# Optimization experiments

Hardware: AMD Instinct MI355X
Metric: run time of the kernel (lower is better)

The kernel has to match this reference:

```python
import jax, jax.numpy as jnp
import numpy as np

N_NODES = 100000
N_EDGES = 1600000
IN_DIM, HIDDEN, OUT_DIM = 128, 64, 32


def setup_inputs() -> dict:
    key = jax.random.key(0)
    k1, k2, k3, k4 = jax.random.split(key, 4)
    x = jax.random.normal(k1, (N_NODES, IN_DIM), dtype=jnp.float32)
    # Glorot-style init for the two GCN linear layers
    W1 = jax.random.normal(k2, (IN_DIM, HIDDEN), dtype=jnp.float32) * (1.0 / np.sqrt(IN_DIM))
    b1 = jnp.zeros((HIDDEN,), dtype=jnp.float32)
    W2 = jax.random.normal(k3, (HIDDEN, OUT_DIM), dtype=jnp.float32) * (1.0 / np.sqrt(HIDDEN))
    b2 = jnp.zeros((OUT_DIM,), dtype=jnp.float32)
    edge_index = jax.random.randint(k4, (2, N_EDGES), 0, N_NODES, dtype=jnp.int32)
    return {"x": x, "W1": W1, "b1": b1, "W2": W2, "b2": b2, "edge_index": edge_index}


def _gcn_norm(edge_index, n_nodes):
    # Add self-loops and compute symmetric normalization D^{-1/2} (A+I) D^{-1/2}
    loops = jnp.arange(n_nodes, dtype=edge_index.dtype)
    src = jnp.concatenate([edge_index[0], loops])  # [E+N]
    dst = jnp.concatenate([edge_index[1], loops])
    deg = jax.ops.segment_sum(jnp.ones_like(dst, dtype=jnp.float32), dst,
                              num_segments=n_nodes)
    dinv = jnp.where(deg > 0, jax.lax.rsqrt(deg), 0.0)
    norm = dinv[src] * dinv[dst]  # [E+N]
    return src, dst, norm


def _gcn_conv(h, W, b, src, dst, norm, n_nodes):
    h = h @ W                                   # [N, out] linear transform first
    msg = h[src] * norm[:, None]                # gather + per-edge scale
    agg = jax.ops.segment_sum(msg, dst, num_segments=n_nodes)  # scatter-add
    return agg + b


def reference(x, W1, b1, W2, b2, edge_index):
    n = x.shape[0]
    src, dst, norm = _gcn_norm(edge_index, n)
    h = jax.nn.relu(_gcn_conv(x, W1, b1, src, dst, norm, n))
    # dropout is identity in eval mode (deterministic reference)
    z = _gcn_conv(h, W2, b2, src, dst, norm, n)
    return z
```

## Files before the change

### kernel.cpp

```cpp
#include <hip/hip_runtime.h>
#include <hip/hip_fp16.h>

#define NB_MAX 784
#define CAP    2560
#define CHUNK  8192

typedef _Float16 half8 __attribute__((ext_vector_type(8)));
typedef float f32x4_t __attribute__((ext_vector_type(4)));

__global__ __launch_bounds__(256) void k_bin_gemm1(
        const int* __restrict__ src, const int* __restrict__ dst,
        int* __restrict__ gcur, int* __restrict__ binned, int nb, int e,
        const float* __restrict__ x, const float* __restrict__ W1,
        __half* __restrict__ hp, int n, int binb) {
    __shared__ __align__(16) char smem[64 * 136 * 2];
    const int t = threadIdx.x;

    if (blockIdx.x < binb) {
        int* hist = (int*)smem;
        int* curs = hist + NB_MAX;
        const int base = blockIdx.x * CHUNK;
        const int lim = min(CHUNK, e - base);

        for (int i = t; i < NB_MAX; i += 256) hist[i] = 0;
        __syncthreads();

        const int i4lim = lim >> 2;
        for (int i = t; i < i4lim; i += 256) {
            int4 d = ((const int4*)(dst + base))[i];
            atomicAdd(&hist[d.x >> 7], 1);
            atomicAdd(&hist[d.y >> 7], 1);
            atomicAdd(&hist[d.z >> 7], 1);
            atomicAdd(&hist[d.w >> 7], 1);
        }
        for (int i = (i4lim << 2) + t; i < lim; i += 256)
            atomicAdd(&hist[dst[base + i] >> 7], 1);
        __syncthreads();

        for (int b = t; b < nb; b += 256) {
            int h = hist[b];
            curs[b] = h ? atomicAdd(&gcur[b], h) : 0;
        }
        __syncthreads();

        for (int i = t; i < i4lim; i += 256) {
            int4 d = ((const int4*)(dst + base))[i];
            int4 s = ((const int4*)(src + base))[i];
            int o0 = atomicAdd(&curs[d.x >> 7], 1);
            int o1 = atomicAdd(&curs[d.y >> 7], 1);
            int o2 = atomicAdd(&curs[d.z >> 7], 1);
            int o3 = atomicAdd(&curs[d.w >> 7], 1);
            if (o0 < CAP) binned[(size_t)(d.x >> 7) * CAP + o0] = (s.x << 7) | (d.x & 127);
            if (o1 < CAP) binned[(size_t)(d.y >> 7) * CAP + o1] = (s.y << 7) | (d.y & 127);
            if (o2 < CAP) binned[(size_t)(d.z >> 7) * CAP + o2] = (s.z << 7) | (d.z & 127);
            if (o3 < CAP) binned[(size_t)(d.w >> 7) * CAP + o3] = (s.w << 7) | (d.w & 127);
        }
        for (int i = (i4lim << 2) + t; i < lim; i += 256) {
            int d = dst[base + i], s = src[base + i];
            int off = atomicAdd(&curs[d >> 7], 1);
            if (off < CAP) binned[(size_t)(d >> 7) * CAP + off] = (s << 7) | (d & 127);
        }
        return;
    }

    _Float16* wt = (_Float16*)smem;

    for (int i = t; i < 128 * 64; i += 256) {
        int k = i >> 6, o = i & 63;
        wt[o * 136 + k] = (_Float16)W1[i];
    }
    __syncthreads();

    const int lane = t & 63;
    const int wid  = t >> 6;
    const int row0 = (blockIdx.x - binb) * 64 + wid * 16;
    const int rA   = lane & 15;
    const int g    = lane >> 4;

    f32x4_t acc0 = {0.f, 0.f, 0.f, 0.f};
    f32x4_t acc1 = {0.f, 0.f, 0.f, 0.f};
    f32x4_t acc2 = {0.f, 0.f, 0.f, 0.f};
    f32x4_t acc3 = {0.f, 0.f, 0.f, 0.f};

    const int arow = min(row0 + rA, n - 1);
    const float* ap0 = x + (size_t)arow * 128 + g * 8;

#pragma unroll
    for (int ks = 0; ks < 4; ++ks) {
        const float* ap = ap0 + ks * 32;
        float4 a0 = *(const float4*)ap;
        float4 a1 = *(const float4*)(ap + 4);
        half8 af;
        af[0] = (_Float16)a0.x; af[1] = (_Float16)a0.y;
        af[2] = (_Float16)a0.z; af[3] = (_Float16)a0.w;
        af[4] = (_Float16)a1.x; af[5] = (_Float16)a1.y;
        af[6] = (_Float16)a1.z; af[7] = (_Float16)a1.w;

        const _Float16* wb = wt + rA * 136 + ks * 32 + g * 8;
        half8 b0 = *(const half8*)(wb);
        half8 b1 = *(const half8*)(wb + 16 * 136);
        half8 b2 = *(const half8*)(wb + 32 * 136);
        half8 b3 = *(const half8*)(wb + 48 * 136);
        acc0 = __builtin_amdgcn_mfma_f32_16x16x32_f16(af, b0, acc0, 0, 0, 0);
        acc1 = __builtin_amdgcn_mfma_f32_16x16x32_f16(af, b1, acc1, 0, 0, 0);
        acc2 = __builtin_amdgcn_mfma_f32_16x16x32_f16(af, b2, acc2, 0, 0, 0);
        acc3 = __builtin_amdgcn_mfma_f32_16x16x32_f16(af, b3, acc3, 0, 0, 0);
    }

    _Float16* hph = (_Float16*)hp;
#pragma unroll
    for (int r = 0; r < 4; ++r) {
        int node = row0 + g * 4 + r;
        if (node >= n) continue;
        _Float16* o = hph + (size_t)node * 64 + rA;
        o[0]  = (_Float16)acc0[r];
        o[16] = (_Float16)acc1[r];
        o[32] = (_Float16)acc2[r];
        o[48] = (_Float16)acc3[r];
    }
}

__global__ __launch_bounds__(1024) void k_base(const int* __restrict__ gcur,
                                               int* __restrict__ cbase,
                                               int* __restrict__ rpx,
                                               int nb, int n, int e) {
    __shared__ int sm[1024];
    int t = threadIdx.x;
    int v = (t < nb) ? gcur[t] : 0;
    sm[t] = v;
    __syncthreads();
    for (int o = 1; o < 1024; o <<= 1) {
        int add = (t >= o) ? sm[t - o] : 0;
        __syncthreads();
        sm[t] += add;
        __syncthreads();
    }
    if (t < nb) cbase[t] = sm[t] - v;
    if (t == 0) rpx[n] = e;
}

__global__ __launch_bounds__(256) void k_sort(const int* __restrict__ binned,
                                              const int* __restrict__ gcur,
                                              const int* __restrict__ cbase,
                                              int* __restrict__ csr,
                                              int* __restrict__ rpx,
                                              float* __restrict__ dinv, int n) {
    __shared__ int hist[128], offs[128];
    const int t = threadIdx.x;
    const int b = blockIdx.x;
    if (t < 128) hist[t] = 0;
    __syncthreads();

    int sz = gcur[b];
    if (sz > CAP) sz = CAP;
    const int* bp = binned + (size_t)b * CAP;

    const int i4 = sz >> 2;
    for (int i = t; i < i4; i += 256) {
        int4 p = ((const int4*)bp)[i];
        atomicAdd(&hist[p.x & 127], 1);
        atomicAdd(&hist[p.y & 127], 1);
        atomicAdd(&hist[p.z & 127], 1);
        atomicAdd(&hist[p.w & 127], 1);
    }
    for (int i = (i4 << 2) + t; i < sz; i += 256)
        atomicAdd(&hist[bp[i] & 127], 1);
    __syncthreads();

    if (t < 128) offs[t] = hist[t];
    __syncthreads();
    for (int o = 1; o < 128; o <<= 1) {
        int add = (t < 128 && t >= o) ? offs[t - o] : 0;
        __syncthreads();
        if (t < 128) offs[t] += add;
        __syncthreads();
    }

    const int base = cbase[b];
    if (t < 128) {
        int node = (b << 7) + t;
        if (node < n) {
            rpx[node]  = base + offs[t] - hist[t];
            dinv[node] = rsqrtf(1.0f + (float)hist[t]);
        }
    }
    __syncthreads();
    if (t < 128) hist[t] = offs[t] - hist[t];
    __syncthreads();

    for (int i = t; i < sz; i += 256) {
        int p = bp[i];
        int pos = base + atomicAdd(&hist[p & 127], 1);
        csr[pos] = p >> 7;
    }
}


union Pk8 { float4 f4; __half2 h2[4]; };

__device__ inline void addrow(float acc[8], float4 v) {
    Pk8 u; u.f4 = v;
#pragma unroll
    for (int j = 0; j < 4; ++j) {
        float2 t = __half22float2(u.h2[j]);
        acc[2 * j]     += t.x;
        acc[2 * j + 1] += t.y;
    }
}

__device__ inline void addrow_s(float acc[8], float4 v, float s) {
    Pk8 u; u.f4 = v;
#pragma unroll
    for (int j = 0; j < 4; ++j) {
        float2 t = __half22float2(u.h2[j]);
        acc[2 * j]     = fmaf(t.x, s, acc[2 * j]);
        acc[2 * j + 1] = fmaf(t.y, s, acc[2 * j + 1]);
    }
}

__global__ __launch_bounds__(256) void k_agg1(const int* __restrict__ rpx,
                                              const int* __restrict__ csr,
                                              const __half* __restrict__ hp,
                                              const float* __restrict__ dinv,
                                              const float* __restrict__ b1,
                                              const float* __restrict__ W2,
                                              __half* __restrict__ hp2, int n) {
    __shared__ float w2t[32 * 68];
    __shared__ float tl[32 * 68];
    const int t = threadIdx.x;

    for (int i = t; i < 64 * 32; i += 256) {
        int f = i >> 5, j = i & 31;
        w2t[j * 68 + f] = W2[i];
    }

    const int nl   = t >> 3;
    const int q    = t & 7;
    const int node = blockIdx.x * 32 + nl;
    const bool alive = node < n;

    float acc[8];
#pragma unroll
    for (int j = 0; j < 8; ++j) acc[j] = 0.f;

    float di = 0.f;
    if (alive) {
        const float4* hp4 = (const float4*)hp;
        int start = rpx[node], end = rpx[node + 1];
        di = dinv[node];
        addrow_s(acc, hp4[(size_t)node * 8 + q], di);

        int p = start;
        for (; p + 8 <= end; p += 8) {
            int s[8];
#pragma unroll
            for (int j = 0; j < 8; ++j) s[j] = csr[p + j];
            float ds[8];
#pragma unroll
            for (int j = 0; j < 8; ++j) ds[j] = dinv[s[j]];
            float4 v[8];
#pragma unroll
            for (int j = 0; j < 8; ++j) v[j] = hp4[(size_t)s[j] * 8 + q];
#pragma unroll
            for (int j = 0; j < 8; ++j) addrow_s(acc, v[j], ds[j]);
        }
        for (; p + 2 <= end; p += 2) {
            int s0 = csr[p], s1 = csr[p + 1];
            float d0 = dinv[s0], d1 = dinv[s1];
            float4 v0 = hp4[(size_t)s0 * 8 + q];
            float4 v1 = hp4[(size_t)s1 * 8 + q];
            addrow_s(acc, v0, d0);
            addrow_s(acc, v1, d1);
        }
        if (p < end) {
            int s0 = csr[p];
            addrow_s(acc, hp4[(size_t)s0 * 8 + q], dinv[s0]);
        }
    }

    float4 ba = ((const float4*)b1)[q * 2];
    float4 bb = ((const float4*)b1)[q * 2 + 1];
    float4 t0, t1;
    t0.x = fmaxf(fmaf(acc[0], di, ba.x), 0.f);
    t0.y = fmaxf(fmaf(acc[1], di, ba.y), 0.f);
    t0.z = fmaxf(fmaf(acc[2], di, ba.z), 0.f);
    t0.w = fmaxf(fmaf(acc[3], di, ba.w), 0.f);
    t1.x = fmaxf(fmaf(acc[4], di, bb.x), 0.f);
    t1.y = fmaxf(fmaf(acc[5], di, bb.y), 0.f);
    t1.z = fmaxf(fmaf(acc[6], di, bb.z), 0.f);
    t1.w = fmaxf(fmaf(acc[7], di, bb.w), 0.f);
    *(float4*)(tl + nl * 68 + q * 8)     = t0;
    *(float4*)(tl + nl * 68 + q * 8 + 4) = t1;
    __syncthreads();

    if (!alive) return;

    const float* trow = tl + nl * 68;
    const float* wa = w2t + q * 68;
    const float* wb = w2t + (q + 8) * 68;
    const float* wc = w2t + (q + 16) * 68;
    const float* wd = w2t + (q + 24) * 68;
    float o0 = 0.f, o1 = 0.f, o2 = 0.f, o3 = 0.f;
#pragma unroll
    for (int f4 = 0; f4 < 16; ++f4) {
        float4 tv = *(const float4*)(trow + f4 * 4);
        float4 v0 = *(const float4*)(wa + f4 * 4);
        float4 v1 = *(const float4*)(wb + f4 * 4);
        float4 v2 = *(const float4*)(wc + f4 * 4);
        float4 v3 = *(const float4*)(wd + f4 * 4);
        o0 += tv.x * v0.x + tv.y * v0.y + tv.z * v0.z + tv.w * v0.w;
        o1 += tv.x * v1.x + tv.y * v1.y + tv.z * v1.z + tv.w * v1.w;
        o2 += tv.x * v2.x + tv.y * v2.y + tv.z * v2.z + tv.w * v2.w;
        o3 += tv.x * v3.x + tv.y * v3.y + tv.z * v3.z + tv.w * v3.w;
    }
    _Float16* hq = (_Float16*)hp2 + (size_t)node * 32;
    hq[q]      = (_Float16)(o0 * di);
    hq[q + 8]  = (_Float16)(o1 * di);
    hq[q + 16] = (_Float16)(o2 * di);
    hq[q + 24] = (_Float16)(o3 * di);
}

template<int LOGF>
__global__ __launch_bounds__(256) void k_aggregate(const int* __restrict__ rpx,
                                                   const int* __restrict__ csr,
                                                   const __half* __restrict__ hp,
                                                   const float* __restrict__ dinv,
                                                   const float* __restrict__ bias,
                                                   float* __restrict__ out, int n) {
    constexpr int F   = 1 << LOGF;
    constexpr int TPN = F / 8;
    int gid  = blockIdx.x * 256 + threadIdx.x;
    int node = gid / TPN;
    int q    = gid % TPN;
    if (node >= n) return;

    const float4* hp4 = (const float4*)hp;
    int start = rpx[node], end = rpx[node + 1];

    float acc[8];
#pragma unroll
    for (int j = 0; j < 8; ++j) acc[j] = 0.f;
    addrow(acc, hp4[(size_t)node * TPN + q]);

    int p = start;
    for (; p + 8 <= end; p += 8) {
        int s[8];
#pragma unroll
        for (int j = 0; j < 8; ++j) s[j] = csr[p + j];
        float4 v[8];
#pragma unroll
        for (int j = 0; j < 8; ++j) v[j] = hp4[(size_t)s[j] * TPN + q];
#pragma unroll
        for (int j = 0; j < 8; ++j) addrow(acc, v[j]);
    }
    for (; p + 2 <= end; p += 2) {
        int s0 = csr[p], s1 = csr[p + 1];
        float4 v0 = hp4[(size_t)s0 * TPN + q];
        float4 v1 = hp4[(size_t)s1 * TPN + q];
        addrow(acc, v0);
        addrow(acc, v1);
    }
    if (p < end)
        addrow(acc, hp4[(size_t)csr[p] * TPN + q]);

    float di = dinv[node];
    float4 b0 = ((const float4*)bias)[q * 2];
    float4 b1v = ((const float4*)bias)[q * 2 + 1];
    float4 r0, r1;
    r0.x = fmaf(acc[0], di, b0.x); r0.y = fmaf(acc[1], di, b0.y);
    r0.z = fmaf(acc[2], di, b0.z); r0.w = fmaf(acc[3], di, b0.w);
    r1.x = fmaf(acc[4], di, b1v.x); r1.y = fmaf(acc[5], di, b1v.y);
    r1.z = fmaf(acc[6], di, b1v.z); r1.w = fmaf(acc[7], di, b1v.w);
    float4* o4 = (float4*)out;
    o4[(size_t)node * (F / 4) + q * 2]     = r0;
    o4[(size_t)node * (F / 4) + q * 2 + 1] = r1;
}


extern "C" void kernel_launch(void* const* d_in, const int* in_sizes, int n_in,
                              void* d_out, int out_size, void* d_ws, size_t ws_size,
                              hipStream_t stream) {
    const float* x  = (const float*)d_in[0];
    const float* W1 = (const float*)d_in[1];
    const float* b1 = (const float*)d_in[2];
    const float* W2 = (const float*)d_in[3];
    const float* b2 = (const float*)d_in[4];
    const int*   ei = (const int*)d_in[5];

    const int N = in_sizes[0] / 128;
    const int E = in_sizes[5] / 2;
    const int* src = ei;
    const int* dst = ei + E;
    const int NB = (N + 127) >> 7;

    char* w = (char*)d_ws;
    int*    gcur   = (int*)w;                  w += NB_MAX * 4;
    int*    cbase  = (int*)w;                  w += NB_MAX * 4;
    int*    rpx    = (int*)w;                  w += (size_t)(N + 4) * 4;
    float*  dinv   = (float*)w;                w += (size_t)N * 4;
    int*    binned = (int*)w;                  w += (size_t)NB_MAX * CAP * 4;
    int*    csr    = (int*)w;                  w += (size_t)E * 4;
    __half* hp     = (__half*)w;               w += (size_t)N * 64 * 2;
    __half* hp2    = (__half*)w;               w += (size_t)N * 32 * 2;
    float*  out    = (float*)d_out;

    const int binb = (E + CHUNK - 1) / CHUNK;
    const int gb1  = (N + 63) / 64;

    hipMemsetAsync(gcur, 0, NB_MAX * 4, stream);

    k_bin_gemm1<<<binb + gb1, 256, 0, stream>>>(src, dst, gcur, binned, NB, E,
                                                x, W1, hp, N, binb);

    k_base<<<1, 1024, 0, stream>>>(gcur, cbase, rpx, NB, N, E);
    k_sort<<<NB, 256, 0, stream>>>(binned, gcur, cbase, csr, rpx, dinv, N);

    k_agg1<<<(N + 31) / 32, 256, 0, stream>>>(rpx, csr, hp, dinv, b1, W2, hp2, N);

    k_aggregate<5><<<(N * 4 + 255) / 256, 256, 0, stream>>>(rpx, csr, hp2, dinv, b2, out, N);
}
```

Before: 136.4 us.

## Fold bin prefix scan into sort kernel and use nontemporal streaming loads

Removes the separate single-block prefix-scan kernel. Each sort block now sums the counts of all preceding bins itself with a block reduction, which saves one kernel launch and its serialization point at the cost of some redundant reads of the small count array. It also switches streaming reads of edge, bin and CSR data, plus the final output stores, to nontemporal loads and stores to reduce cache pollution.

Result: slower. 146.3 us (+7.2%).

```diff
diff --git a/kernel.cpp b/kernel.cpp
--- a/kernel.cpp
+++ b/kernel.cpp
@@ -7,6 +7,10 @@
 
 typedef _Float16 half8 __attribute__((ext_vector_type(8)));
 typedef float f32x4_t __attribute__((ext_vector_type(4)));
+typedef int   i32x4   __attribute__((ext_vector_type(4)));
+
+__device__ inline int   ntld (const int*   p) { return __builtin_nontemporal_load(p); }
+__device__ inline i32x4 ntld4(const int*   p) { return __builtin_nontemporal_load((const i32x4*)p); }
 
 __global__ __launch_bounds__(256) void k_bin_gemm1(
         const int* __restrict__ src, const int* __restrict__ dst,
@@ -44,8 +48,8 @@
         __syncthreads();
 
         for (int i = t; i < i4lim; i += 256) {
-            int4 d = ((const int4*)(dst + base))[i];
-            int4 s = ((const int4*)(src + base))[i];
+            i32x4 d = ntld4(dst + base + i * 4);
+            i32x4 s = ntld4(src + base + i * 4);
             int o0 = atomicAdd(&curs[d.x >> 7], 1);
             int o1 = atomicAdd(&curs[d.y >> 7], 1);
             int o2 = atomicAdd(&curs[d.z >> 7], 1);
@@ -120,36 +124,28 @@
     }
 }
 
-__global__ __launch_bounds__(1024) void k_base(const int* __restrict__ gcur,
-                                               int* __restrict__ cbase,
-                                               int* __restrict__ rpx,
-                                               int nb, int n, int e) {
-    __shared__ int sm[1024];
-    int t = threadIdx.x;
-    int v = (t < nb) ? gcur[t] : 0;
-    sm[t] = v;
-    __syncthreads();
-    for (int o = 1; o < 1024; o <<= 1) {
-        int add = (t >= o) ? sm[t - o] : 0;
-        __syncthreads();
-        sm[t] += add;
-        __syncthreads();
-    }
-    if (t < nb) cbase[t] = sm[t] - v;
-    if (t == 0) rpx[n] = e;
-}
-
 __global__ __launch_bounds__(256) void k_sort(const int* __restrict__ binned,
                                               const int* __restrict__ gcur,
-                                              const int* __restrict__ cbase,
                                               int* __restrict__ csr,
                                               int* __restrict__ rpx,
-                                              float* __restrict__ dinv, int n) {
+                                              float* __restrict__ dinv,
+                                              int n, int e) {
     __shared__ int hist[128], offs[128];
+    __shared__ int red[256];
     const int t = threadIdx.x;
     const int b = blockIdx.x;
+
+    int partial = 0;
+    for (int j = t; j < b; j += 256) partial += gcur[j];
+    red[t] = partial;
     if (t < 128) hist[t] = 0;
     __syncthreads();
+    for (int o = 128; o > 0; o >>= 1) {
+        if (t < o) red[t] += red[t + o];
+        __syncthreads();
+    }
+    const int base = red[0];
+    if (b == 0 && t == 0) rpx[n] = e;
 
     int sz = gcur[b];
     if (sz > CAP) sz = CAP;
@@ -157,14 +153,14 @@
 
     const int i4 = sz >> 2;
     for (int i = t; i < i4; i += 256) {
-        int4 p = ((const int4*)bp)[i];
+        i32x4 p = ntld4(bp + i * 4);
         atomicAdd(&hist[p.x & 127], 1);
         atomicAdd(&hist[p.y & 127], 1);
         atomicAdd(&hist[p.z & 127], 1);
         atomicAdd(&hist[p.w & 127], 1);
     }
     for (int i = (i4 << 2) + t; i < sz; i += 256)
-        atomicAdd(&hist[bp[i] & 127], 1);
+        atomicAdd(&hist[ntld(bp + i) & 127], 1);
     __syncthreads();
 
     if (t < 128) offs[t] = hist[t];
@@ -176,7 +172,6 @@
         __syncthreads();
     }
 
-    const int base = cbase[b];
     if (t < 128) {
         int node = (b << 7) + t;
         if (node < n) {
@@ -189,7 +184,7 @@
     __syncthreads();
 
     for (int i = t; i < sz; i += 256) {
-        int p = bp[i];
+        int p = ntld(bp + i);
         int pos = base + atomicAdd(&hist[p & 127], 1);
         csr[pos] = p >> 7;
     }
@@ -254,7 +249,7 @@
         for (; p + 8 <= end; p += 8) {
             int s[8];
 #pragma unroll
-            for (int j = 0; j < 8; ++j) s[j] = csr[p + j];
+            for (int j = 0; j < 8; ++j) s[j] = ntld(csr + p + j);
             float ds[8];
 #pragma unroll
             for (int j = 0; j < 8; ++j) ds[j] = dinv[s[j]];
@@ -265,7 +260,7 @@
             for (int j = 0; j < 8; ++j) addrow_s(acc, v[j], ds[j]);
         }
         for (; p + 2 <= end; p += 2) {
-            int s0 = csr[p], s1 = csr[p + 1];
+            int s0 = ntld(csr + p), s1 = ntld(csr + p + 1);
             float d0 = dinv[s0], d1 = dinv[s1];
             float4 v0 = hp4[(size_t)s0 * 8 + q];
             float4 v1 = hp4[(size_t)s1 * 8 + q];
@@ -273,7 +268,7 @@
             addrow_s(acc, v1, d1);
         }
         if (p < end) {
-            int s0 = csr[p];
+            int s0 = ntld(csr + p);
             addrow_s(acc, hp4[(size_t)s0 * 8 + q], dinv[s0]);
         }
     }
@@ -346,7 +341,7 @@
     for (; p + 8 <= end; p += 8) {
         int s[8];
 #pragma unroll
-        for (int j = 0; j < 8; ++j) s[j] = csr[p + j];
+        for (int j = 0; j < 8; ++j) s[j] = ntld(csr + p + j);
         float4 v[8];
 #pragma unroll
         for (int j = 0; j < 8; ++j) v[j] = hp4[(size_t)s[j] * TPN + q];
@@ -354,26 +349,26 @@
         for (int j = 0; j < 8; ++j) addrow(acc, v[j]);
     }
     for (; p + 2 <= end; p += 2) {
-        int s0 = csr[p], s1 = csr[p + 1];
+        int s0 = ntld(csr + p), s1 = ntld(csr + p + 1);
         float4 v0 = hp4[(size_t)s0 * TPN + q];
         float4 v1 = hp4[(size_t)s1 * TPN + q];
         addrow(acc, v0);
         addrow(acc, v1);
     }
     if (p < end)
-        addrow(acc, hp4[(size_t)csr[p] * TPN + q]);
+        addrow(acc, hp4[(size_t)ntld(csr + p) * TPN + q]);
 
     float di = dinv[node];
     float4 b0 = ((const float4*)bias)[q * 2];
     float4 b1v = ((const float4*)bias)[q * 2 + 1];
-    float4 r0, r1;
+    f32x4_t r0, r1;
     r0.x = fmaf(acc[0], di, b0.x); r0.y = fmaf(acc[1], di, b0.y);
     r0.z = fmaf(acc[2], di, b0.z); r0.w = fmaf(acc[3], di, b0.w);
     r1.x = fmaf(acc[4], di, b1v.x); r1.y = fmaf(acc[5], di, b1v.y);
     r1.z = fmaf(acc[6], di, b1v.z); r1.w = fmaf(acc[7], di, b1v.w);
-    float4* o4 = (float4*)out;
-    o4[(size_t)node * (F / 4) + q * 2]     = r0;
-    o4[(size_t)node * (F / 4) + q * 2 + 1] = r1;
+    f32x4_t* o4 = (f32x4_t*)out;
+    __builtin_nontemporal_store(r0, o4 + (size_t)node * (F / 4) + q * 2);
+    __builtin_nontemporal_store(r1, o4 + (size_t)node * (F / 4) + q * 2 + 1);
 }
 
 
@@ -395,7 +390,6 @@
 
     char* w = (char*)d_ws;
     int*    gcur   = (int*)w;                  w += NB_MAX * 4;
-    int*    cbase  = (int*)w;                  w += NB_MAX * 4;
     int*    rpx    = (int*)w;                  w += (size_t)(N + 4) * 4;
     float*  dinv   = (float*)w;                w += (size_t)N * 4;
     int*    binned = (int*)w;                  w += (size_t)NB_MAX * CAP * 4;
@@ -407,13 +401,12 @@
     const int binb = (E + CHUNK - 1) / CHUNK;
     const int gb1  = (N + 63) / 64;
 
-    hipMemsetAsync(gcur, 0, NB_MAX * 4, stream);
+    (void)hipMemsetAsync(gcur, 0, NB_MAX * 4, stream);
 
     k_bin_gemm1<<<binb + gb1, 256, 0, stream>>>(src, dst, gcur, binned, NB, E,
                                                 x, W1, hp, N, binb);
 
-    k_base<<<1, 1024, 0, stream>>>(gcur, cbase, rpx, NB, N, E);
-    k_sort<<<NB, 256, 0, stream>>>(binned, gcur, cbase, csr, rpx, dinv, N);
+    k_sort<<<NB, 256, 0, stream>>>(binned, gcur, csr, rpx, dinv, N, E);
 
     k_agg1<<<(N + 31) / 32, 256, 0, stream>>>(rpx, csr, hp, dinv, b1, W2, hp2, N);
 
```
